# Optimization experiments

Measured on AMD Instinct MI355X. Metric: run time of the kernel, lower is better.

## Reference

```python
import jax, jax.numpy as jnp
import numpy as np

N_NODES = 100000
N_EDGES = 1000000
D_IN = 64
D_HID = 64
D_OUT = 1


def setup_inputs() -> dict:
    key = jax.random.key(0)
    ks = jax.random.split(key, 10)
    s = 1.0 / np.sqrt(D_IN)
    x = jax.random.normal(ks[0], (N_NODES, D_IN), dtype=jnp.float32)
    edge_index = jax.random.randint(ks[1], (2, N_EDGES), 0, N_NODES, dtype=jnp.int64)
    return {
        "x": x,
        "edge_index": edge_index,
        "W_rel0": jax.random.normal(ks[2], (D_HID, D_IN), dtype=jnp.float32) * s,
        "b_rel0": jax.random.normal(ks[3], (D_HID,), dtype=jnp.float32) * s,
        "W_root0": jax.random.normal(ks[4], (D_HID, D_IN), dtype=jnp.float32) * s,
        "W_rel1": jax.random.normal(ks[5], (D_HID, D_HID), dtype=jnp.float32) * s,
        "b_rel1": jax.random.normal(ks[6], (D_HID,), dtype=jnp.float32) * s,
        "W_root1": jax.random.normal(ks[7], (D_HID, D_HID), dtype=jnp.float32) * s,
        "W_out": jax.random.normal(ks[8], (D_OUT, D_HID), dtype=jnp.float32) * s,
        "b_out": jax.random.normal(ks[9], (D_OUT,), dtype=jnp.float32) * s,
    }


def graph_conv(x, src, dst, W_rel, b_rel, W_root):
    # PyG GraphConv (aggr='add'): out_i = W_rel @ sum_{j->i} x_j + b_rel + W_root @ x_i
    # transform-then-aggregate == aggregate-then-transform; aggregate first (smaller GEMM input)
    agg = jax.ops.segment_sum(x[src], dst, num_segments=N_NODES)  # [N, d]
    return agg @ W_rel.T + b_rel + x @ W_root.T


def reference(x, edge_index, W_rel0, b_rel0, W_root0, W_rel1, b_rel1, W_root1, W_out, b_out):
    src, dst = edge_index[0], edge_index[1]
    h = jnp.tanh(graph_conv(x, src, dst, W_rel0, b_rel0, W_root0))
    # F.dropout(training=self.training) is identity in eval mode
    h = jnp.tanh(graph_conv(h, src, dst, W_rel1, b_rel1, W_root1))
    return h @ W_out.T + b_out  # [N, output_dim]
```

## Files before the change

kernel.cpp:

```cpp
#include <hip/hip_runtime.h>
#include <math.h>

#define D 64
#define BCAP 4096

typedef unsigned short u16;
typedef unsigned int u32;
typedef __attribute__((ext_vector_type(8))) short short8v;
typedef __attribute__((ext_vector_type(4))) float f32x4;

__device__ __forceinline__ float asf(u32 u) {
    union { u32 u; float f; } t; t.u = u; return t.f;
}
__device__ __forceinline__ u16 f2bf(float f) {
    union { float ff; u32 u; } t; t.ff = f;
    u32 r = t.u + 0x7FFF + ((t.u >> 16) & 1);
    return (u16)(r >> 16);
}
#define BF_LO(p) asf((p) << 16)
#define BF_HI(p) asf((p) & 0xFFFF0000u)

__device__ __forceinline__ int block_detect_i64(const u32* ei2, int n_edges) {
    __shared__ u32 wred[8];
    int cap = n_edges < 2048 ? n_edges : 2048;
    u32 v = 0;
    for (int i = threadIdx.x; i < cap; i += blockDim.x) v |= ei2[2 * i + 1];
    #pragma unroll
    for (int off = 32; off > 0; off >>= 1) v |= __shfl_down(v, off);
    if ((threadIdx.x & 63) == 0) wred[threadIdx.x >> 6] = v;
    __syncthreads();
    u32 o = 0;
    int nw = (blockDim.x + 63) >> 6;
    for (int k = 0; k < nw; ++k) o |= wred[k];
    __syncthreads();
    return o == 0;
}

__device__ __forceinline__ int load_dst(const void* ei, int f64, int n_edges, int e) {
    return f64 ? (int)((const long long*)ei)[(size_t)n_edges + e]
               : ((const int*)ei)[(size_t)n_edges + e];
}
__device__ __forceinline__ int load_src(const void* ei, int f64, int e) {
    return f64 ? (int)((const long long*)ei)[e] : ((const int*)ei)[e];
}

__global__ __launch_bounds__(256) void prep_kernel(
        const float* __restrict__ x, u16* __restrict__ xb, int n4,
        const float* __restrict__ Wr0, const float* __restrict__ Wt0,
        const float* __restrict__ Wr1, const float* __restrict__ Wt1,
        u16* __restrict__ wb, int* __restrict__ bcur16, int NB) {
    int gid = blockIdx.x * 256 + threadIdx.x;
    int gsz = gridDim.x * 256;
    for (int i = gid; i < n4; i += gsz) {
        float4 v = *(const float4*)(x + (size_t)i * 4);
        ushort4 o;
        o.x = f2bf(v.x); o.y = f2bf(v.y); o.z = f2bf(v.z); o.w = f2bf(v.w);
        *(ushort4*)(xb + (size_t)i * 4) = o;
    }
    for (int i = gid; i < 4096; i += gsz) {
        int wsel = i >> 10, g = i & 1023;
        const float* W = (wsel == 0) ? Wr0 : (wsel == 1) ? Wt0
                        : (wsel == 2) ? Wr1 : Wt1;
        float4 v = *(const float4*)(W + g * 4);
        ushort4 o;
        o.x = f2bf(v.x); o.y = f2bf(v.y); o.z = f2bf(v.z); o.w = f2bf(v.w);
        *(ushort4*)(wb + wsel * 4096 + g * 4) = o;
    }
    for (int b = gid; b < NB; b += gsz) bcur16[b * 16] = b * BCAP;
}

__global__ __launch_bounds__(512) void part_kernel(
        const void* __restrict__ ei,
        int* __restrict__ bcur16, uint2* __restrict__ pairs,
        int n_edges, int NB) {
    __shared__ int h[512], lb[512], gb[512], cur[512];
    __shared__ int part[512];
    __shared__ uint2 stage[4096];

    int f64 = block_detect_i64((const u32*)ei, n_edges);
    int t = threadIdx.x;
    int tile0 = blockIdx.x * 4096;
    int cnt = n_edges - tile0; if (cnt > 4096) cnt = 4096;

    for (int i = t; i < 512; i += 512) h[i] = 0;
    __syncthreads();
    for (int i = t; i < cnt; i += 512)
        atomicAdd(&h[load_dst(ei, f64, n_edges, tile0 + i) >> 8], 1);
    __syncthreads();
    {
        int v = h[t];
        part[t] = v;
        __syncthreads();
        for (int off = 1; off < 512; off <<= 1) {
            int u = (t >= off) ? part[t - off] : 0;
            __syncthreads();
            part[t] += u;
            __syncthreads();
        }
        lb[t] = part[t] - v;
        cur[t] = part[t] - v;
    }
    for (int b = t; b < NB; b += 512)
        gb[b] = h[b] ? atomicAdd(&bcur16[b * 16], h[b]) : 0;
    __syncthreads();
    for (int i = t; i < cnt; i += 512) {
        int s = load_src(ei, f64, tile0 + i);
        int d = load_dst(ei, f64, n_edges, tile0 + i);
        int r = atomicAdd(&cur[d >> 8], 1);
        stage[r] = make_uint2((u32)d, (u32)s);
    }
    __syncthreads();
    for (int i = t; i < cnt; i += 512) {
        uint2 p = stage[i];
        int b = (int)(p.x >> 8);
        pairs[(size_t)gb[b] + (i - lb[b])] = p;
    }
}

__global__ __launch_bounds__(256) void bucket_kernel(
        const uint2* __restrict__ pairs, const int* __restrict__ bcur16,
        int2* __restrict__ rowse, int* __restrict__ col, int n_nodes) {
    __shared__ int cnt[256], lb[256], cur[256], part[256];
    __shared__ u32 colst[BCAP];

    int t = threadIdx.x;
    int b = blockIdx.x;
    int base = b * BCAP;
    int span = bcur16[b * 16] - base;
    if (span > BCAP) span = BCAP;
    int node0 = b << 8;

    cnt[t] = 0;
    __syncthreads();
    for (int i = t; i < span; i += 256)
        atomicAdd(&cnt[pairs[base + i].x - node0], 1);
    __syncthreads();
    {
        int v = cnt[t];
        part[t] = v;
        __syncthreads();
        for (int off = 1; off < 256; off <<= 1) {
            int u = (t >= off) ? part[t - off] : 0;
            __syncthreads();
            part[t] += u;
            __syncthreads();
        }
        lb[t] = part[t] - v;
        cur[t] = part[t] - v;
    }
    if (node0 + t < n_nodes)
        rowse[node0 + t] = make_int2(base + lb[t], base + lb[t] + cnt[t]);
    __syncthreads();
    for (int i = t; i < span; i += 256) {
        uint2 p = pairs[base + i];
        int r = atomicAdd(&cur[p.x - node0], 1);
        colst[r] = p.y;
    }
    __syncthreads();
    for (int i = t; i < span; i += 256)
        col[base + i] = (int)colst[i];
}

__device__ __forceinline__ void g4(const u32* __restrict__ xrow,
                                   const int* __restrict__ col, int e, int c,
                                   float& a0, float& a1, float& a2, float& a3) {
    int s0 = col[e], s1 = col[e + 1], s2 = col[e + 2], s3 = col[e + 3];
    uint2 v0 = *(const uint2*)(xrow + (size_t)s0 * 32 + c * 2);
    uint2 v1 = *(const uint2*)(xrow + (size_t)s1 * 32 + c * 2);
    uint2 v2 = *(const uint2*)(xrow + (size_t)s2 * 32 + c * 2);
    uint2 v3 = *(const uint2*)(xrow + (size_t)s3 * 32 + c * 2);
    a0 += (BF_LO(v0.x) + BF_LO(v1.x)) + (BF_LO(v2.x) + BF_LO(v3.x));
    a1 += (BF_HI(v0.x) + BF_HI(v1.x)) + (BF_HI(v2.x) + BF_HI(v3.x));
    a2 += (BF_LO(v0.y) + BF_LO(v1.y)) + (BF_LO(v2.y) + BF_LO(v3.y));
    a3 += (BF_HI(v0.y) + BF_HI(v1.y)) + (BF_HI(v2.y) + BF_HI(v3.y));
}
__device__ __forceinline__ void gtail(const u32* __restrict__ xrow,
                                      const int* __restrict__ col, int e, int end,
                                      int c, float& a0, float& a1, float& a2,
                                      float& a3) {
    if (e >= end) return;
    int last = end - 1;
    int i1 = (e + 1 < last) ? e + 1 : last;
    int i2 = (e + 2 < last) ? e + 2 : last;
    int s0 = col[e], s1 = col[i1], s2 = col[i2];
    uint2 v0 = *(const uint2*)(xrow + (size_t)s0 * 32 + c * 2);
    uint2 v1 = *(const uint2*)(xrow + (size_t)s1 * 32 + c * 2);
    uint2 v2 = *(const uint2*)(xrow + (size_t)s2 * 32 + c * 2);
    float m1 = (e + 1 < end) ? 1.f : 0.f;
    float m2 = (e + 2 < end) ? 1.f : 0.f;
    a0 += BF_LO(v0.x); a1 += BF_HI(v0.x); a2 += BF_LO(v0.y); a3 += BF_HI(v0.y);
    a0 = fmaf(m1, BF_LO(v1.x), a0); a1 = fmaf(m1, BF_HI(v1.x), a1);
    a2 = fmaf(m1, BF_LO(v1.y), a2); a3 = fmaf(m1, BF_HI(v1.y), a3);
    a0 = fmaf(m2, BF_LO(v2.x), a0); a1 = fmaf(m2, BF_HI(v2.x), a1);
    a2 = fmaf(m2, BF_LO(v2.y), a2); a3 = fmaf(m2, BF_HI(v2.y), a3);
}

template <bool OUT_HEAD>
__global__ __launch_bounds__(512, 8) void layer_kernel(
        const u16* __restrict__ xin,
        const int2* __restrict__ rowse, const int* __restrict__ col,
        const u16* __restrict__ wbR, const u16* __restrict__ wbT,
        const float* __restrict__ brel,
        const float* __restrict__ Wout, const float* __restrict__ bout,
        void* __restrict__ outp, int n_nodes) {
    __shared__ u16 aggL[64 * 64];
    __shared__ u16 xL[64 * 64];
    __shared__ float part[4][64];

    int tid = threadIdx.x;
    int w = tid >> 6;
    int lane = tid & 63;
    int q = lane >> 4;
    int c = lane & 15;

    int base = blockIdx.x * 64;
    int nlocA = w * 8 + q * 2;
    int nlocB = nlocA + 1;
    int nodeA = base + nlocA;
    int nodeB = base + nlocB;
    bool vA = nodeA < n_nodes;
    bool vB = nodeB < n_nodes;
    int2 seA = vA ? rowse[nodeA] : make_int2(0, 0);
    int2 seB = vB ? rowse[nodeB] : make_int2(0, 0);

    const u32* xrow = (const u32*)xin;

    uint2 xrA = make_uint2(0u, 0u), xrB = make_uint2(0u, 0u);
    if (vA) xrA = *(const uint2*)(xrow + (size_t)nodeA * 32 + c * 2);
    if (vB) xrB = *(const uint2*)(xrow + (size_t)nodeB * 32 + c * 2);

    float a0 = 0.f, a1 = 0.f, a2 = 0.f, a3 = 0.f;
    float b0 = 0.f, b1 = 0.f, b2 = 0.f, b3 = 0.f;
    int eA = seA.x, eB = seB.x;
    while (eA + 4 <= seA.y && eB + 4 <= seB.y) {
        g4(xrow, col, eA, c, a0, a1, a2, a3);
        g4(xrow, col, eB, c, b0, b1, b2, b3);
        eA += 4; eB += 4;
    }
    for (; eA + 4 <= seA.y; eA += 4) g4(xrow, col, eA, c, a0, a1, a2, a3);
    for (; eB + 4 <= seB.y; eB += 4) g4(xrow, col, eB, c, b0, b1, b2, b3);
    gtail(xrow, col, eA, seA.y, c, a0, a1, a2, a3);
    gtail(xrow, col, eB, seB.y, c, b0, b1, b2, b3);

    {
        u32 offA = (u32)nlocA * 128 + (((u32)c * 8) ^ (((u32)nlocA & 7) << 4));
        u32 offB = (u32)nlocB * 128 + (((u32)c * 8) ^ (((u32)nlocB & 7) << 4));
        uint2 apA = make_uint2((u32)f2bf(a0) | ((u32)f2bf(a1) << 16),
                               (u32)f2bf(a2) | ((u32)f2bf(a3) << 16));
        uint2 apB = make_uint2((u32)f2bf(b0) | ((u32)f2bf(b1) << 16),
                               (u32)f2bf(b2) | ((u32)f2bf(b3) << 16));
        *(uint2*)((char*)aggL + offA) = apA;
        *(uint2*)((char*)xL + offA) = xrA;
        *(uint2*)((char*)aggL + offB) = apB;
        *(uint2*)((char*)xL + offB) = xrB;
    }

    int ftile = w & 3;
    int nt0 = (w >> 2) * 2;
    int mrow = lane & 15;
    int kblk = lane >> 4;
    int j = ftile * 16 + mrow;
    short8v bR0 = *(const short8v*)(wbR + j * 64 + kblk * 8);
    short8v bR1 = *(const short8v*)(wbR + j * 64 + kblk * 8 + 32);
    short8v bT0 = *(const short8v*)(wbT + j * 64 + kblk * 8);
    short8v bT1 = *(const short8v*)(wbT + j * 64 + kblk * 8 + 32);
    float bias = brel[j];
    float wj = OUT_HEAD ? Wout[j] : 0.f;

    __syncthreads();

    for (int t = 0; t < 2; ++t) {
        int ntile = nt0 + t;
        int arow = ntile * 16 + mrow;
        u32 mask = ((u32)arow & 7) << 4;
        u32 off0 = (u32)arow * 128 + (((u32)kblk * 16) ^ mask);
        u32 off1 = (u32)arow * 128 + (((u32)kblk * 16 + 64) ^ mask);
        short8v aA0 = *(const short8v*)((const char*)aggL + off0);
        short8v aA1 = *(const short8v*)((const char*)aggL + off1);
        short8v aX0 = *(const short8v*)((const char*)xL + off0);
        short8v aX1 = *(const short8v*)((const char*)xL + off1);

        f32x4 acc = {0.f, 0.f, 0.f, 0.f};
        acc = __builtin_amdgcn_mfma_f32_16x16x32_bf16(aA0, bR0, acc, 0, 0, 0);
        acc = __builtin_amdgcn_mfma_f32_16x16x32_bf16(aA1, bR1, acc, 0, 0, 0);
        acc = __builtin_amdgcn_mfma_f32_16x16x32_bf16(aX0, bT0, acc, 0, 0, 0);
        acc = __builtin_amdgcn_mfma_f32_16x16x32_bf16(aX1, bT1, acc, 0, 0, 0);

        float h0 = tanhf(acc[0] + bias);
        float h1 = tanhf(acc[1] + bias);
        float h2 = tanhf(acc[2] + bias);
        float h3 = tanhf(acc[3] + bias);

        int orow = base + ntile * 16 + kblk * 4;
        if (OUT_HEAD) {
            float v0 = h0 * wj, v1 = h1 * wj, v2 = h2 * wj, v3 = h3 * wj;
            #pragma unroll
            for (int off = 1; off < 16; off <<= 1) {
                v0 += __shfl_xor(v0, off);
                v1 += __shfl_xor(v1, off);
                v2 += __shfl_xor(v2, off);
                v3 += __shfl_xor(v3, off);
            }
            if (mrow == 0) {
                int rl = ntile * 16 + kblk * 4;
                part[ftile][rl + 0] = v0;
                part[ftile][rl + 1] = v1;
                part[ftile][rl + 2] = v2;
                part[ftile][rl + 3] = v3;
            }
        } else {
            u16* out = (u16*)outp;
            if (orow + 0 < n_nodes) out[(size_t)(orow + 0) * D + j] = f2bf(h0);
            if (orow + 1 < n_nodes) out[(size_t)(orow + 1) * D + j] = f2bf(h1);
            if (orow + 2 < n_nodes) out[(size_t)(orow + 2) * D + j] = f2bf(h2);
            if (orow + 3 < n_nodes) out[(size_t)(orow + 3) * D + j] = f2bf(h3);
        }
    }

    if (OUT_HEAD) {
        __syncthreads();
        if (tid < 64) {
            int n = base + tid;
            if (n < n_nodes) {
                float* out = (float*)outp;
                out[n] = part[0][tid] + part[1][tid] + part[2][tid] +
                         part[3][tid] + bout[0];
            }
        }
    }
}

extern "C" void kernel_launch(void* const* d_in, const int* in_sizes, int n_in,
                              void* d_out, int out_size, void* d_ws, size_t ws_size,
                              hipStream_t stream) {
    const float* x      = (const float*)d_in[0];
    const void*  ei     = d_in[1];
    const float* Wrel0  = (const float*)d_in[2];
    const float* brel0  = (const float*)d_in[3];
    const float* Wroot0 = (const float*)d_in[4];
    const float* Wrel1  = (const float*)d_in[5];
    const float* brel1  = (const float*)d_in[6];
    const float* Wroot1 = (const float*)d_in[7];
    const float* Wout   = (const float*)d_in[8];
    const float* bout   = (const float*)d_in[9];
    float* out = (float*)d_out;

    const int n_nodes = in_sizes[0] / D;
    const int n_edges = in_sizes[1] / 2;
    const int NB = (n_nodes + 255) >> 8;

    u16*   xb     = (u16*)d_ws;
    u16*   hb     = xb + (size_t)n_nodes * D;
    u16*   wb     = hb + (size_t)n_nodes * D;
    uint2* pairs  = (uint2*)(wb + 4 * 4096);
    int*   col    = (int*)(pairs + (size_t)NB * BCAP);
    int2*  rowse  = (int2*)(col + (size_t)NB * BCAP);
    int*   bcur16 = (int*)(rowse + n_nodes);

    const int n4 = n_nodes * D / 4;

    prep_kernel<<<512, 256, 0, stream>>>(x, xb, n4, Wrel0, Wroot0, Wrel1,
                                         Wroot1, wb, bcur16, NB);
    part_kernel<<<(n_edges + 4095) / 4096, 512, 0, stream>>>(
        ei, bcur16, pairs, n_edges, NB);
    bucket_kernel<<<NB, 256, 0, stream>>>(pairs, bcur16, rowse, col, n_nodes);

    const int nlb = (n_nodes + 63) / 64;
    layer_kernel<false><<<nlb, 512, 0, stream>>>(
        xb, rowse, col, wb, wb + 4096, brel0, nullptr, nullptr, hb, n_nodes);
    layer_kernel<true><<<nlb, 512, 0, stream>>>(
        hb, rowse, col, wb + 2 * 4096, wb + 3 * 4096, brel1, Wout, bout,
        out, n_nodes);
}
```

Measured before the change: 105.0 us.

## Fuse prep into edge partitioning and replace global bucket atomics with per-tile run table

Merges the bf16 conversion prep kernel into the edge partition kernel, dropping one launch. Partitioned edges are now packed into 32-bit words (src<<8 | dst&255) and written in place per tile. Each tile also records per-bucket offsets in a run table, which removes the global atomic slot reservation. The bucket kernel then walks every tile's run for its bucket, so each bucket block reads from 245 scattered tile segments, with serial per-thread loops over runs. Packing src into 24 bits limits node count to 16M, and the run table stores only 512 entries per tile, so the b+1 read assumes NB < 512.

After: 104.4 us. No clear change (-0.5%).

```diff
diff --git a/kernel.cpp b/kernel.cpp
--- a/kernel.cpp
+++ b/kernel.cpp
@@ -3,6 +3,8 @@
 
 #define D 64
 #define BCAP 4096
+#define TILE 4096
+#define NBP  512
 
 typedef unsigned short u16;
 typedef unsigned int u32;
@@ -44,13 +46,21 @@
     return f64 ? (int)((const long long*)ei)[e] : ((const int*)ei)[e];
 }
 
-__global__ __launch_bounds__(256) void prep_kernel(
+__global__ __launch_bounds__(512) void part_prep_kernel(
+        const void* __restrict__ ei, u32* __restrict__ pairs,
+        u16* __restrict__ runtab,
         const float* __restrict__ x, u16* __restrict__ xb, int n4,
         const float* __restrict__ Wr0, const float* __restrict__ Wt0,
         const float* __restrict__ Wr1, const float* __restrict__ Wt1,
-        u16* __restrict__ wb, int* __restrict__ bcur16, int NB) {
-    int gid = blockIdx.x * 256 + threadIdx.x;
-    int gsz = gridDim.x * 256;
+        u16* __restrict__ wb, int n_edges) {
+    __shared__ int h[512], lb[512], cur[512], part[512];
+    __shared__ u32 stage[TILE];
+
+    int f64 = block_detect_i64((const u32*)ei, n_edges);
+    int t = threadIdx.x;
+    int gid = blockIdx.x * 512 + t;
+    int gsz = gridDim.x * 512;
+
     for (int i = gid; i < n4; i += gsz) {
         float4 v = *(const float4*)(x + (size_t)i * 4);
         ushort4 o;
@@ -66,21 +76,10 @@
         o.x = f2bf(v.x); o.y = f2bf(v.y); o.z = f2bf(v.z); o.w = f2bf(v.w);
         *(ushort4*)(wb + wsel * 4096 + g * 4) = o;
     }
-    for (int b = gid; b < NB; b += gsz) bcur16[b * 16] = b * BCAP;
-}
-
-__global__ __launch_bounds__(512) void part_kernel(
-        const void* __restrict__ ei,
-        int* __restrict__ bcur16, uint2* __restrict__ pairs,
-        int n_edges, int NB) {
-    __shared__ int h[512], lb[512], gb[512], cur[512];
-    __shared__ int part[512];
-    __shared__ uint2 stage[4096];
-
-    int f64 = block_detect_i64((const u32*)ei, n_edges);
-    int t = threadIdx.x;
-    int tile0 = blockIdx.x * 4096;
-    int cnt = n_edges - tile0; if (cnt > 4096) cnt = 4096;
+
+    int tile0 = blockIdx.x * TILE;
+    int cnt = n_edges - tile0; if (cnt > TILE) cnt = TILE;
+    if (cnt <= 0) return;
 
     for (int i = t; i < 512; i += 512) h[i] = 0;
     __syncthreads();
@@ -100,40 +99,40 @@
         lb[t] = part[t] - v;
         cur[t] = part[t] - v;
     }
-    for (int b = t; b < NB; b += 512)
-        gb[b] = h[b] ? atomicAdd(&bcur16[b * 16], h[b]) : 0;
+    runtab[(size_t)blockIdx.x * NBP + t] = (u16)lb[t];
     __syncthreads();
     for (int i = t; i < cnt; i += 512) {
         int s = load_src(ei, f64, tile0 + i);
         int d = load_dst(ei, f64, n_edges, tile0 + i);
         int r = atomicAdd(&cur[d >> 8], 1);
-        stage[r] = make_uint2((u32)d, (u32)s);
-    }
-    __syncthreads();
-    for (int i = t; i < cnt; i += 512) {
-        uint2 p = stage[i];
-        int b = (int)(p.x >> 8);
-        pairs[(size_t)gb[b] + (i - lb[b])] = p;
-    }
+        stage[r] = ((u32)s << 8) | ((u32)d & 255u);
+    }
+    __syncthreads();
+    for (int i = t; i < cnt; i += 512)
+        pairs[tile0 + i] = stage[i];
 }
 
 __global__ __launch_bounds__(256) void bucket_kernel(
-        const uint2* __restrict__ pairs, const int* __restrict__ bcur16,
-        int2* __restrict__ rowse, int* __restrict__ col, int n_nodes) {
+        const u32* __restrict__ pairs, const u16* __restrict__ runtab,
+        int2* __restrict__ rowse, int* __restrict__ col,
+        int n_nodes, int ntiles) {
     __shared__ int cnt[256], lb[256], cur[256], part[256];
+    __shared__ int sTotal;
     __shared__ u32 colst[BCAP];
 
     int t = threadIdx.x;
     int b = blockIdx.x;
     int base = b * BCAP;
-    int span = bcur16[b * 16] - base;
-    if (span > BCAP) span = BCAP;
     int node0 = b << 8;
 
     cnt[t] = 0;
     __syncthreads();
-    for (int i = t; i < span; i += 256)
-        atomicAdd(&cnt[pairs[base + i].x - node0], 1);
+    for (int tt = t; tt < ntiles; tt += 256) {
+        int off0 = runtab[(size_t)tt * NBP + b];
+        int off1 = runtab[(size_t)tt * NBP + b + 1];
+        for (int i = off0; i < off1; ++i)
+            atomicAdd(&cnt[pairs[tt * TILE + i] & 255u], 1);
+    }
     __syncthreads();
     {
         int v = cnt[t];
@@ -147,16 +146,22 @@
         }
         lb[t] = part[t] - v;
         cur[t] = part[t] - v;
+        if (t == 255) sTotal = part[255];
     }
     if (node0 + t < n_nodes)
         rowse[node0 + t] = make_int2(base + lb[t], base + lb[t] + cnt[t]);
     __syncthreads();
-    for (int i = t; i < span; i += 256) {
-        uint2 p = pairs[base + i];
-        int r = atomicAdd(&cur[p.x - node0], 1);
-        colst[r] = p.y;
-    }
-    __syncthreads();
+    for (int tt = t; tt < ntiles; tt += 256) {
+        int off0 = runtab[(size_t)tt * NBP + b];
+        int off1 = runtab[(size_t)tt * NBP + b + 1];
+        for (int i = off0; i < off1; ++i) {
+            u32 p = pairs[tt * TILE + i];
+            int r = atomicAdd(&cur[p & 255u], 1);
+            if (r < BCAP) colst[r] = p >> 8;
+        }
+    }
+    __syncthreads();
+    int span = sTotal; if (span > BCAP) span = BCAP;
     for (int i = t; i < span; i += 256)
         col[base + i] = (int)colst[i];
 }
@@ -348,22 +353,23 @@
     const int n_nodes = in_sizes[0] / D;
     const int n_edges = in_sizes[1] / 2;
     const int NB = (n_nodes + 255) >> 8;
-
-    u16*   xb     = (u16*)d_ws;
+    const int nt = (n_edges + TILE - 1) / TILE;
+
+    int2*  rowse  = (int2*)d_ws;
+    u32*   pairs  = (u32*)(rowse + n_nodes);
+    int*   col    = (int*)(pairs + (size_t)nt * TILE);
+    u16*   runtab = (u16*)(col + (size_t)NB * BCAP);
+    u16*   xb     = runtab + (size_t)nt * NBP;
     u16*   hb     = xb + (size_t)n_nodes * D;
     u16*   wb     = hb + (size_t)n_nodes * D;
-    uint2* pairs  = (uint2*)(wb + 4 * 4096);
-    int*   col    = (int*)(pairs + (size_t)NB * BCAP);
-    int2*  rowse  = (int2*)(col + (size_t)NB * BCAP);
-    int*   bcur16 = (int*)(rowse + n_nodes);
 
     const int n4 = n_nodes * D / 4;
 
-    prep_kernel<<<512, 256, 0, stream>>>(x, xb, n4, Wrel0, Wroot0, Wrel1,
-                                         Wroot1, wb, bcur16, NB);
-    part_kernel<<<(n_edges + 4095) / 4096, 512, 0, stream>>>(
-        ei, bcur16, pairs, n_edges, NB);
-    bucket_kernel<<<NB, 256, 0, stream>>>(pairs, bcur16, rowse, col, n_nodes);
+    part_prep_kernel<<<nt, 512, 0, stream>>>(
+        ei, pairs, runtab, x, xb, n4, Wrel0, Wroot0, Wrel1, Wroot1, wb,
+        n_edges);
+    bucket_kernel<<<NB, 256, 0, stream>>>(pairs, runtab, rowse, col,
+                                          n_nodes, nt);
 
     const int nlb = (n_nodes + 63) / 64;
     layer_kernel<false><<<nlb, 512, 0, stream>>>(
```
